# Kernel optimization log

Measured on AMD Instinct MI355X. Metric: run time of the kernel, lower is better.

The kernel has to match this reference:

```python
import jax, jax.numpy as jnp
import numpy as np

N = 6144          # num utterances (graph nodes)
D = 128           # utt_embed_size
WIN = 10          # att_window_size
NUM_SPK = 8
N_EMO = 7


def _init(key, shape):
    fan_in = shape[0]
    return jax.random.normal(key, shape, dtype=jnp.float32) * (1.0 / np.sqrt(fan_in))


def setup_inputs() -> dict:
    key = jax.random.key(0)
    ks = jax.random.split(key, 20)
    inp = {
        "x": jax.random.normal(ks[0], (N, D), dtype=jnp.float32),
        "speakers": jax.random.randint(ks[1], (N,), 0, NUM_SPK, dtype=jnp.int32),
        # layer-1 relation GCN weights (pred / suc / same / diff)
        "W_pred1": _init(ks[2], (D, D)),
        "W_suc1": _init(ks[3], (D, D)),
        "W_same1": _init(ks[4], (D, D)),
        "W_diff1": _init(ks[5], (D, D)),
        # layer-2 relation GCN weights
        "W_pred2": _init(ks[6], (D, D)),
        "W_suc2": _init(ks[7], (D, D)),
        "W_same2": _init(ks[8], (D, D)),
        "W_diff2": _init(ks[9], (D, D)),
        "w_aggr_1": _init(ks[10], (D, D)),
        "w_aggr_2": _init(ks[11], (D, D)),
        "w_e1": _init(ks[12], (2 * D, D)),
        "b_e1": jnp.zeros((D,), dtype=jnp.float32),
        "w_e2": _init(ks[13], (D, N_EMO)),
        "b_e2": jnp.zeros((N_EMO,), dtype=jnp.float32),
        "w_s": _init(ks[14], (2 * D, N_EMO)),
        "b_s": jnp.zeros((N_EMO,), dtype=jnp.float32),
    }
    return inp


def reference(x, speakers, W_pred1, W_suc1, W_same1, W_diff1,
              W_pred2, W_suc2, W_same2, W_diff2,
              w_aggr_1, w_aggr_2, w_e1, b_e1, w_e2, b_e2, w_s, b_s):
    n = x.shape[0]
    idx = jnp.arange(n)
    # windowed dot-product attention; entries outside the window stay 0.0
    # BEFORE the softmax (faithful to the torch code: zeros, not -inf)
    band = jnp.abs(idx[:, None] - idx[None, :]) <= WIN
    scores = jnp.where(band, x @ x.T, 0.0)            # [N, N]
    attn = jax.nn.softmax(scores, axis=1)
    # relation masks
    same = (speakers[:, None] == speakers[None, :]).astype(x.dtype)
    pred = (idx[None, :] >= idx[:, None]).astype(x.dtype)   # triu incl diag
    suc = 1.0 - pred                                          # strict lower tri
    adjs = (same * pred * attn,        # same-speaker, predecessor
            same * suc * attn,         # same-speaker, successor
            (1.0 - same) * pred * attn,  # diff-speaker, predecessor
            (1.0 - same) * suc * attn)   # diff-speaker, successor

    def gcn(h, Ws):  # sum_k adj_k @ (h @ W_k)
        return sum(a @ (h @ w) for a, w in zip(adjs, Ws))

    d = jnp.diagonal(attn)[:, None]   # self-attention scale
    h1 = jax.nn.relu(gcn(x, (W_pred1, W_suc1, W_same1, W_diff1))
                     + (x @ w_aggr_1) * d)
    h2 = jax.nn.relu(gcn(h1, (W_pred2, W_suc2, W_same2, W_diff2))
                     + (h1 @ w_aggr_2) * d)
    h = jnp.concatenate([h2, x], axis=1)              # [N, 2D]
    emotion = jax.nn.relu(h @ w_e1 + b_e1) @ w_e2 + b_e2   # [N, 7]
    sentiment = h @ w_s + b_s                               # [N, 7]
    return emotion, sentiment
```

## Files before the change

### kernel.cpp

```cpp
#include <hip/hip_runtime.h>
#include <hip/hip_bf16.h>


#define NN   6144
#define DD   128
#define WINW 10
#define YST  168
#define TAB_OFF 27456
#define SS_OFF  33088
#define SM_BYTES 35904
#define NBLK 768
#define WS_W1T 0
#define WS_W2T 163840
#define WS_WE1 327680
#define WS_WE2 393216
#define WS_WST 397312
#define WS_H1  405504
#define WS_H2  1978368
#define BAR_OFF 3551232
#define F1_OFF 16384
#define F2_OFF 40960
#define BAR_BYTES 65536

typedef unsigned short u16;
typedef unsigned long long u64;
typedef __attribute__((ext_vector_type(8))) short bf16x8;
typedef __attribute__((ext_vector_type(4))) float f32x4;

__device__ __forceinline__ float b2f(u16 u) {
    return __uint_as_float(((unsigned int)u) << 16);
}
__device__ __forceinline__ u16 f2b(float f) {
    __hip_bfloat16 h = __float2bfloat16(f);
    return *reinterpret_cast<u16*>(&h);
}
__device__ __forceinline__ bf16x8 cvt8(const float* p) {
    float4 u = *reinterpret_cast<const float4*>(p);
    float4 v = *reinterpret_cast<const float4*>(p + 4);
    bf16x8 r;
    r[0] = (short)f2b(u.x); r[1] = (short)f2b(u.y);
    r[2] = (short)f2b(u.z); r[3] = (short)f2b(u.w);
    r[4] = (short)f2b(v.x); r[5] = (short)f2b(v.y);
    r[6] = (short)f2b(v.z); r[7] = (short)f2b(v.w);
    return r;
}
__device__ __forceinline__ void st_agent_u32(unsigned* p, unsigned v) {
    __hip_atomic_store(p, v, __ATOMIC_RELAXED, __HIP_MEMORY_SCOPE_AGENT);
}
__device__ __forceinline__ void st_agent_u64(u64* p, u64 v) {
    __hip_atomic_store(p, v, __ATOMIC_RELAXED, __HIP_MEMORY_SCOPE_AGENT);
}
__device__ __forceinline__ unsigned ld_agent_u32(const unsigned* p) {
    return __hip_atomic_load(p, __ATOMIC_RELAXED, __HIP_MEMORY_SCOPE_AGENT);
}
__device__ __forceinline__ unsigned add_agent_u32(unsigned* p, unsigned v) {
    return __hip_atomic_fetch_add(p, v, __ATOMIC_RELAXED,
                                  __HIP_MEMORY_SCOPE_AGENT);
}
__device__ __forceinline__ void poll_ge(unsigned* p, unsigned v) {
    while (ld_agent_u32(p) < v) __builtin_amdgcn_s_sleep(1);
}
__device__ __forceinline__ const float* sel5(int r,
    const float* a0, const float* a1, const float* a2,
    const float* a3, const float* a4) {
    return r == 0 ? a0 : r == 1 ? a1 : r == 2 ? a2 : r == 3 ? a3 : a4;
}

__device__ __forceinline__ void layer_tile(
    const float* __restrict__ x, const u16* __restrict__ Ab16,
    const u16* __restrict__ BT, const int* __restrict__ spk,
    u16* __restrict__ hout, int first_layer, int hb, int bm,
    char* smraw, int tid, char* gate, int bid)
{
    u16*   Ys  = (u16*)smraw;
    float* Xs  = (float*)smraw;
    int2*  tab = (int2*)(smraw + TAB_OFF);
    float* Ss  = (float*)(smraw + SS_OFF);
    const int wave = tid >> 6, lane = tid & 63;
    const int lm = lane & 15, quad = lane >> 4;
    const int wm = wave >> 1, wn = wave & 1;

    bf16x8 afr[2][4];

    if (first_layer) {
        #pragma unroll
        for (int it = 0; it < 7; ++it) {
            int f = tid + it * 256;
            if (f < 52 * 32) {
                int s = f >> 5, c = f & 31;
                int g = min(max(bm - WINW + s, 0), NN - 1);
                *reinterpret_cast<float4*>(&Xs[s * 132 + c * 4]) =
                    *reinterpret_cast<const float4*>(&x[(size_t)g * DD + c * 4]);
            }
        }
        __syncthreads();

        if (tid < 128) {
            const int il = tid >> 2, q = tid & 3;
            const float* xr = &Xs[(il + WINW) * 132 + q * 32];
            float4 xq[8];
            #pragma unroll
            for (int c = 0; c < 8; ++c) {
                int cc = (c + 2 * q) & 7;
                xq[c] = *reinterpret_cast<const float4*>(xr + cc * 4);
            }
            float po[21];
            #pragma unroll
            for (int o = 0; o < 21; ++o) {
                const float* jr = &Xs[(il + o) * 132 + q * 32];
                float a0 = 0.f, a1 = 0.f, a2 = 0.f, a3 = 0.f;
                #pragma unroll
                for (int c = 0; c < 8; ++c) {
                    int cc = (c + 2 * q) & 7;
                    float4 b = *reinterpret_cast<const float4*>(jr + cc * 4);
                    a0 = fmaf(xq[c].x, b.x, a0); a1 = fmaf(xq[c].y, b.y, a1);
                    a2 = fmaf(xq[c].z, b.z, a2); a3 = fmaf(xq[c].w, b.w, a3);
                }
                po[o] = (a0 + a1) + (a2 + a3);
            }
            #pragma unroll
            for (int o = 0; o < 21; ++o) {
                po[o] += __shfl_xor(po[o], 1);
                po[o] += __shfl_xor(po[o], 2);
            }
            if (q == 0) {
                #pragma unroll
                for (int o = 0; o < 21; ++o) {
                    int jg = bm + il - WINW + o;
                    Ss[il * 22 + o] =
                        (jg >= 0 && jg < NN) ? po[o] : -1e30f;
                }
            }
        }
        __syncthreads();

        if (tid < 32) {
            int il = tid, i = bm + il;
            float m = 0.f;
            #pragma unroll
            for (int o = 0; o < 21; ++o) {
                float s = Ss[il * 22 + o];
                if (s > -1e29f) m = fmaxf(m, s);
            }
            int lo = i - WINW; if (lo < 0) lo = 0;
            int hi = i + WINW; if (hi > NN - 1) hi = NN - 1;
            float Z = (float)(NN - (hi - lo + 1)) * __expf(-m);
            float ev[21];
            #pragma unroll
            for (int o = 0; o < 21; ++o) {
                float s = Ss[il * 22 + o];
                ev[o] = (s > -1e29f) ? __expf(s - m) : 0.f;
                Z += ev[o];
            }
            float rz = 1.f / Z;
            #pragma unroll
            for (int o = 0; o < 21; ++o) Ss[il * 22 + o] = ev[o] * rz;
        }
        __syncthreads();

        #pragma unroll
        for (int rr = 0; rr < 3; ++rr) {
            int p = tid + rr * 256;
            if (p < 704) {
                int il = p / 22, e = p - il * 22;
                int i  = bm + il;
                int si = spk[i];
                float w; int off;
                if (e < 21) {
                    int j = i - WINW + e;
                    bool valid = (j >= 0) && (j < NN);
                    int jc  = valid ? j : i;
                    int sel = (spk[jc] == si) ? ((j >= i) ? 0 : 1)
                                              : ((j >= i) ? 2 : 3);
                    w   = valid ? Ss[il * 22 + e] : 0.f;
                    off = valid ? (il + e) * YST + sel * 32 : 0;
                } else {
                    w   = Ss[il * 22 + WINW];
                    off = (il + WINW) * YST + 4 * 32;
                }
                tab[p] = make_int2(__float_as_int(w), off);
            }
        }

        #pragma unroll
        for (int mt = 0; mt < 2; ++mt) {
            int rl = min((wm * 2 + mt) * 16 + lm, 51);
            #pragma unroll
            for (int s = 0; s < 4; ++s)
                afr[mt][s] = cvt8(&Xs[rl * 132 + s * 32 + quad * 8]);
        }
        __syncthreads();

        if (gate) {
            if (tid == 0) {
                unsigned g = (unsigned)bid >> 5;
                unsigned* gflag = (unsigned*)(gate + 8192 + g * 128);
                unsigned* rflag = (unsigned*)(gate + 12288);
                if ((bid & 31) == 0) {
                    poll_ge(rflag, 1u);
                    st_agent_u32(gflag, 1u);
                } else {
                    poll_ge(gflag, 1u);
                }
            }
            __syncthreads();
            __builtin_amdgcn_sched_barrier(0);
        }
    } else {
        #pragma unroll
        for (int mt = 0; mt < 2; ++mt) {
            int gr = min(max(bm - WINW + (wm * 2 + mt) * 16 + lm, 0), NN - 1);
            #pragma unroll
            for (int s = 0; s < 4; ++s)
                afr[mt][s] = *reinterpret_cast<const bf16x8*>(
                    Ab16 + (size_t)gr * DD + s * 32 + quad * 8);
        }
    }

    f32x4 acc[2][5];
    #pragma unroll
    for (int mt = 0; mt < 2; ++mt)
        #pragma unroll
        for (int n = 0; n < 5; ++n) acc[mt][n] = {0.f, 0.f, 0.f, 0.f};

    #pragma unroll
    for (int np = 0; np < 5; ++np) {
        int nt = wn * 5 + np;
        int gn = (nt >> 1) * 128 + hb * 32 + (nt & 1) * 16 + lm;
        #pragma unroll
        for (int s = 0; s < 4; ++s) {
            bf16x8 b = *reinterpret_cast<const bf16x8*>(
                BT + (size_t)gn * DD + s * 32 + quad * 8);
            acc[0][np] = __builtin_amdgcn_mfma_f32_16x16x32_bf16(afr[0][s], b, acc[0][np], 0, 0, 0);
            acc[1][np] = __builtin_amdgcn_mfma_f32_16x16x32_bf16(afr[1][s], b, acc[1][np], 0, 0, 0);
        }
    }
    #pragma unroll
    for (int mt = 0; mt < 2; ++mt)
        #pragma unroll
        for (int np = 0; np < 5; ++np) {
            int nt = wn * 5 + np;
            #pragma unroll
            for (int r = 0; r < 4; ++r) {
                int lr = (wm * 2 + mt) * 16 + quad * 4 + r;
                if (lr < 52) Ys[lr * YST + nt * 16 + lm] = f2b(acc[mt][np][r]);
            }
        }
    __syncthreads();

    const int c0 = (tid & 7) * 4;
    const int il = tid >> 3;
    {
        float a0 = 0.f, a1 = 0.f, a2 = 0.f, a3 = 0.f;
        const int2* tp = &tab[il * 22];
        #pragma unroll
        for (int e = 0; e < 22; ++e) {
            int2 t = tp[e];
            float w = __int_as_float(t.x);
            u64 y4 = *reinterpret_cast<const u64*>(Ys + t.y + c0);
            a0 = fmaf(w, b2f((u16)(y4 & 0xffff)), a0);
            a1 = fmaf(w, b2f((u16)((y4 >> 16) & 0xffff)), a1);
            a2 = fmaf(w, b2f((u16)((y4 >> 32) & 0xffff)), a2);
            a3 = fmaf(w, b2f((u16)(y4 >> 48)), a3);
        }
        int i = bm + il;
        u64 pk = (u64)f2b(fmaxf(a0, 0.f)) |
                 ((u64)f2b(fmaxf(a1, 0.f)) << 16) |
                 ((u64)f2b(fmaxf(a2, 0.f)) << 32) |
                 ((u64)f2b(fmaxf(a3, 0.f)) << 48);
        st_agent_u64(reinterpret_cast<u64*>(
            &hout[(size_t)i * DD + hb * 32 + c0]), pk);
    }
}

__global__ __launch_bounds__(256, 4) void fused_kernel(
    const float* __restrict__ x, const int* __restrict__ spk,
    const float* __restrict__ p0, const float* __restrict__ p1,
    const float* __restrict__ p2, const float* __restrict__ p3,
    const float* __restrict__ p4,
    const float* __restrict__ q0, const float* __restrict__ q1,
    const float* __restrict__ q2, const float* __restrict__ q3,
    const float* __restrict__ q4,
    const float* __restrict__ we1, const float* __restrict__ be1,
    const float* __restrict__ we2, const float* __restrict__ be2,
    const float* __restrict__ wss, const float* __restrict__ bss,
    float* __restrict__ out, char* __restrict__ ws)
{
    u16*   W1T   = (u16*)(ws + WS_W1T);
    u16*   W2T   = (u16*)(ws + WS_W2T);
    u16*   We1T  = (u16*)(ws + WS_WE1);
    u16*   we2T  = (u16*)(ws + WS_WE2);
    u16*   wsT   = (u16*)(ws + WS_WST);
    u16*   h1b   = (u16*)(ws + WS_H1);
    u16*   h2b   = (u16*)(ws + WS_H2);
    char*  bar   = ws + BAR_OFF;
    unsigned* flag1 = (unsigned*)(bar + F1_OFF);
    unsigned* flag2 = (unsigned*)(bar + F2_OFF);

    __shared__ __align__(16) char smraw[SM_BYTES];
    const int bid = blockIdx.x;
    const int tid = threadIdx.x;

    if (bid < 160) {
        unsigned* W1T32 = (unsigned*)W1T;
        unsigned* W2T32 = (unsigned*)W2T;
        int idx = bid * 256 + tid;
        int c = idx & 127, rk = idx >> 7;
        int r = rk >> 6, k2 = rk & 63, k = k2 * 2;
        const float* s1 = sel5(r, p0, p1, p2, p3, p4);
        const float* s2 = sel5(r, q0, q1, q2, q3, q4);
        unsigned v1 = (unsigned)f2b(s1[k * 128 + c]) |
                      ((unsigned)f2b(s1[(k + 1) * 128 + c]) << 16);
        unsigned v2 = (unsigned)f2b(s2[k * 128 + c]) |
                      ((unsigned)f2b(s2[(k + 1) * 128 + c]) << 16);
        int U = (r * 128 + c) * 64 + k2;
        st_agent_u32(&W1T32[U], v1);
        st_agent_u32(&W2T32[U], v2);
    } else if (bid < 192) {
        unsigned* We1T32 = (unsigned*)We1T;
        #pragma unroll
        for (int it = 0; it < 2; ++it) {
            int idx = (bid - 160) * 256 + tid + it * 8192;
            int n = idx & 127, k2 = idx >> 7, k = k2 * 2;
            unsigned v = (unsigned)f2b(we1[k * 128 + n]) |
                         ((unsigned)f2b(we1[(k + 1) * 128 + n]) << 16);
            st_agent_u32(&We1T32[n * 128 + k2], v);
        }
    } else if (bid == 192) {
        unsigned* we2T32 = (unsigned*)we2T;
        #pragma unroll
        for (int it = 0; it < 4; ++it) {
            int U = tid + it * 256;
            int n = U >> 6, kh = U & 63, k = kh * 2;
            float lo = n < 7 ? we2[k * 7 + n] : 0.f;
            float hi = n < 7 ? we2[(k + 1) * 7 + n] : 0.f;
            st_agent_u32(&we2T32[U],
                         (unsigned)f2b(lo) | ((unsigned)f2b(hi) << 16));
        }
    } else if (bid == 193) {
        unsigned* wsT32 = (unsigned*)wsT;
        #pragma unroll
        for (int it = 0; it < 8; ++it) {
            int U = tid + it * 256;
            int n = U >> 7, kh = U & 127, k = kh * 2;
            float lo = n < 7 ? wss[k * 7 + n] : 0.f;
            float hi = n < 7 ? wss[(k + 1) * 7 + n] : 0.f;
            st_agent_u32(&wsT32[U],
                         (unsigned)f2b(lo) | ((unsigned)f2b(hi) << 16));
        }
    }

    __syncthreads();
    if (tid == 0) {
        unsigned g = (unsigned)bid >> 5;
        unsigned* gctr = (unsigned*)(bar + g * 128);
        unsigned* rctr = (unsigned*)(bar + 4096);
        unsigned* rflag = (unsigned*)(bar + 12288);
        unsigned r = add_agent_u32(gctr, 1u);
        if (r == 31u) {
            unsigned rr = add_agent_u32(rctr, 1u);
            if (rr == 23u) st_agent_u32(rflag, 1u);
        }
    }

    const int hb = bid / 192, bmi = bid - hb * 192;
    const int bm = bmi * 32;
    layer_tile(x, nullptr, W1T, spk, h1b, 1, hb, bm, smraw, tid, bar, bid);

    __syncthreads();
    if (tid == 0) add_agent_u32(&flag1[bmi * 32], 1u);
    if (tid == 0) {
        if (bmi > 0)   poll_ge(&flag1[(bmi - 1) * 32], 4u);
        poll_ge(&flag1[bmi * 32], 4u);
        if (bmi < 191) poll_ge(&flag1[(bmi + 1) * 32], 4u);
    }
    __syncthreads();
    __builtin_amdgcn_sched_barrier(0);

    layer_tile(nullptr, h1b, W2T, spk, h2b, 0, hb, bm, smraw, tid, nullptr, bid);

    __syncthreads();
    if (tid == 0) add_agent_u32(&flag2[bmi * 32], 1u);

    if (bid < 384) {
        const int rt = (bid & ~15) | ((bid & 7) << 1) | ((bid >> 3) & 1);
        const int bmh = rt * 16;
        if (tid == 0) poll_ge(&flag2[(rt >> 1) * 32], 4u);
        __syncthreads();
        __builtin_amdgcn_sched_barrier(0);

        float* Es = (float*)smraw;
        const int wave = tid >> 6, lane = tid & 63;
        const int lm = lane & 15, quad = lane >> 4;
        const int row = bmh + lm;

        bf16x8 afr[8];
        #pragma unroll
        for (int s = 0; s < 4; ++s)
            afr[s] = *reinterpret_cast<const bf16x8*>(
                &h2b[(size_t)row * DD + s * 32 + quad * 8]);
        #pragma unroll
        for (int s = 4; s < 8; ++s)
            afr[s] = cvt8(&x[(size_t)row * DD + (s - 4) * 32 + quad * 8]);

        f32x4 accE[2], accS = {0.f, 0.f, 0.f, 0.f};
        #pragma unroll
        for (int n = 0; n < 2; ++n) accE[n] = {0.f, 0.f, 0.f, 0.f};

        #pragma unroll
        for (int s = 0; s < 8; ++s) {
            #pragma unroll
            for (int n = 0; n < 2; ++n) {
                int nt = wave * 2 + n;
                bf16x8 b = *reinterpret_cast<const bf16x8*>(
                    &We1T[(size_t)(nt * 16 + lm) * 256 + s * 32 + quad * 8]);
                accE[n] = __builtin_amdgcn_mfma_f32_16x16x32_bf16(afr[s], b, accE[n], 0, 0, 0);
            }
            if (wave == 0) {
                bf16x8 bsf = *reinterpret_cast<const bf16x8*>(
                    &wsT[(size_t)lm * 256 + s * 32 + quad * 8]);
                accS = __builtin_amdgcn_mfma_f32_16x16x32_bf16(afr[s], bsf, accS, 0, 0, 0);
            }
        }

        if (wave == 0 && lm < 7) {
            #pragma unroll
            for (int r = 0; r < 4; ++r) {
                int i = bmh + quad * 4 + r;
                out[(size_t)NN * 7 + (size_t)i * 7 + lm] = accS[r] + bss[lm];
            }
        }
        #pragma unroll
        for (int n = 0; n < 2; ++n) {
            int col = (wave * 2 + n) * 16 + lm;
            float bias = be1[col];
            #pragma unroll
            for (int r = 0; r < 4; ++r)
                Es[(quad * 4 + r) * 132 + col] = fmaxf(accE[n][r] + bias, 0.f);
        }
        __syncthreads();

        if (wave == 0) {
            f32x4 accM = {0.f, 0.f, 0.f, 0.f};
            #pragma unroll
            for (int s = 0; s < 4; ++s) {
                bf16x8 a = cvt8(&Es[lm * 132 + s * 32 + quad * 8]);
                bf16x8 b = *reinterpret_cast<const bf16x8*>(
                    &we2T[(size_t)lm * 128 + s * 32 + quad * 8]);
                accM = __builtin_amdgcn_mfma_f32_16x16x32_bf16(a, b, accM, 0, 0, 0);
            }
            if (lm < 7) {
                #pragma unroll
                for (int r = 0; r < 4; ++r) {
                    int i = bmh + quad * 4 + r;
                    out[(size_t)i * 7 + lm] = accM[r] + be2[lm];
                }
            }
        }
    }
}

extern "C" void kernel_launch(void* const* d_in, const int* in_sizes, int n_in,
                              void* d_out, int out_size, void* d_ws, size_t ws_size,
                              hipStream_t stream)
{
    const float* x   = (const float*)d_in[0];
    const int*   spk = (const int*)d_in[1];
    const float* Wp1 = (const float*)d_in[2];
    const float* Wu1 = (const float*)d_in[3];
    const float* Wm1 = (const float*)d_in[4];
    const float* Wd1 = (const float*)d_in[5];
    const float* Wp2 = (const float*)d_in[6];
    const float* Wu2 = (const float*)d_in[7];
    const float* Wm2 = (const float*)d_in[8];
    const float* Wd2 = (const float*)d_in[9];
    const float* wa1 = (const float*)d_in[10];
    const float* wa2 = (const float*)d_in[11];
    const float* we1 = (const float*)d_in[12];
    const float* be1 = (const float*)d_in[13];
    const float* we2 = (const float*)d_in[14];
    const float* be2 = (const float*)d_in[15];
    const float* wss = (const float*)d_in[16];
    const float* bss = (const float*)d_in[17];
    float* out = (float*)d_out;
    char*  ws  = (char*)d_ws;

    hipMemsetAsync(ws + BAR_OFF, 0, BAR_BYTES, stream);

    fused_kernel<<<dim3(NBLK), dim3(256), 0, stream>>>(
        x, spk, Wp1, Wu1, Wm1, Wd1, wa1, Wp2, Wu2, Wm2, Wd2, wa2,
        we1, be1, we2, be2, wss, bss, out, ws);
}
```

Before: 131.1 us.

## Shrink row tiles to 24 rows and launch 1024 blocks

Cuts the per-block row tile from 32 to 24 rows (44-row halo), raising the grid from 768 to 1024 blocks so more CUs are busy in the persistent fused kernel. The weight-pack readiness barrier is reduced to a single counter over the first 194 blocks instead of a hierarchical count over all blocks. The head-stage tile flags are remapped to the new tile size. In exchange, halo recomputation per useful row rises, and half the waves now issue only one MFMA row tile, so the matrix units are less evenly loaded.

```diff
diff --git a/kernel.cpp b/kernel.cpp
--- a/kernel.cpp
+++ b/kernel.cpp
@@ -5,11 +5,15 @@
 #define NN   6144
 #define DD   128
 #define WINW 10
+#define ROWS 24
+#define HALO 44
+#define NTIL 256
 #define YST  168
-#define TAB_OFF 27456
-#define SS_OFF  33088
-#define SM_BYTES 35904
-#define NBLK 768
+#define TAB_OFF 23232
+#define SS_OFF  27456
+#define SM_BYTES 29568
+#define NBLK 1024
+#define NPACK 194
 #define WS_W1T 0
 #define WS_W2T 163840
 #define WS_WE1 327680
@@ -19,8 +23,8 @@
 #define WS_H2  1978368
 #define BAR_OFF 3551232
 #define F1_OFF 16384
-#define F2_OFF 40960
-#define BAR_BYTES 65536
+#define F2_OFF 49152
+#define BAR_BYTES 81920
 
 typedef unsigned short u16;
 typedef unsigned long long u64;
@@ -79,14 +83,15 @@
     const int wave = tid >> 6, lane = tid & 63;
     const int lm = lane & 15, quad = lane >> 4;
     const int wm = wave >> 1, wn = wave & 1;
+    const int nmt = (wm == 0) ? 2 : 1;
 
     bf16x8 afr[2][4];
 
     if (first_layer) {
         #pragma unroll
-        for (int it = 0; it < 7; ++it) {
+        for (int it = 0; it < 6; ++it) {
             int f = tid + it * 256;
-            if (f < 52 * 32) {
+            if (f < HALO * 32) {
                 int s = f >> 5, c = f & 31;
                 int g = min(max(bm - WINW + s, 0), NN - 1);
                 *reinterpret_cast<float4*>(&Xs[s * 132 + c * 4]) =
@@ -95,15 +100,13 @@
         }
         __syncthreads();
 
-        if (tid < 128) {
+        if (tid < ROWS * 4) {
             const int il = tid >> 2, q = tid & 3;
             const float* xr = &Xs[(il + WINW) * 132 + q * 32];
             float4 xq[8];
             #pragma unroll
-            for (int c = 0; c < 8; ++c) {
-                int cc = (c + 2 * q) & 7;
-                xq[c] = *reinterpret_cast<const float4*>(xr + cc * 4);
-            }
+            for (int c = 0; c < 8; ++c)
+                xq[c] = *reinterpret_cast<const float4*>(xr + c * 4);
             float po[21];
             #pragma unroll
             for (int o = 0; o < 21; ++o) {
@@ -111,8 +114,7 @@
                 float a0 = 0.f, a1 = 0.f, a2 = 0.f, a3 = 0.f;
                 #pragma unroll
                 for (int c = 0; c < 8; ++c) {
-                    int cc = (c + 2 * q) & 7;
-                    float4 b = *reinterpret_cast<const float4*>(jr + cc * 4);
+                    float4 b = *reinterpret_cast<const float4*>(jr + c * 4);
                     a0 = fmaf(xq[c].x, b.x, a0); a1 = fmaf(xq[c].y, b.y, a1);
                     a2 = fmaf(xq[c].z, b.z, a2); a3 = fmaf(xq[c].w, b.w, a3);
                 }
@@ -134,7 +136,7 @@
         }
         __syncthreads();
 
-        if (tid < 32) {
+        if (tid < ROWS) {
             int il = tid, i = bm + il;
             float m = 0.f;
             #pragma unroll
@@ -161,7 +163,7 @@
         #pragma unroll
         for (int rr = 0; rr < 3; ++rr) {
             int p = tid + rr * 256;
-            if (p < 704) {
+            if (p < ROWS * 22) {
                 int il = p / 22, e = p - il * 22;
                 int i  = bm + il;
                 int si = spk[i];
@@ -182,9 +184,8 @@
             }
         }
 
-        #pragma unroll
-        for (int mt = 0; mt < 2; ++mt) {
-            int rl = min((wm * 2 + mt) * 16 + lm, 51);
+        for (int mt = 0; mt < nmt; ++mt) {
+            int rl = min((wm * 2 + mt) * 16 + lm, HALO - 1);
             #pragma unroll
             for (int s = 0; s < 4; ++s)
                 afr[mt][s] = cvt8(&Xs[rl * 132 + s * 32 + quad * 8]);
@@ -195,7 +196,7 @@
             if (tid == 0) {
                 unsigned g = (unsigned)bid >> 5;
                 unsigned* gflag = (unsigned*)(gate + 8192 + g * 128);
-                unsigned* rflag = (unsigned*)(gate + 12288);
+                unsigned* rflag = (unsigned*)(gate + 4096);
                 if ((bid & 31) == 0) {
                     poll_ge(rflag, 1u);
                     st_agent_u32(gflag, 1u);
@@ -207,8 +208,7 @@
             __builtin_amdgcn_sched_barrier(0);
         }
     } else {
-        #pragma unroll
-        for (int mt = 0; mt < 2; ++mt) {
+        for (int mt = 0; mt < nmt; ++mt) {
             int gr = min(max(bm - WINW + (wm * 2 + mt) * 16 + lm, 0), NN - 1);
             #pragma unroll
             for (int s = 0; s < 4; ++s)
@@ -232,25 +232,25 @@
             bf16x8 b = *reinterpret_cast<const bf16x8*>(
                 BT + (size_t)gn * DD + s * 32 + quad * 8);
             acc[0][np] = __builtin_amdgcn_mfma_f32_16x16x32_bf16(afr[0][s], b, acc[0][np], 0, 0, 0);
-            acc[1][np] = __builtin_amdgcn_mfma_f32_16x16x32_bf16(afr[1][s], b, acc[1][np], 0, 0, 0);
-        }
-    }
-    #pragma unroll
-    for (int mt = 0; mt < 2; ++mt)
+            if (wm == 0)
+                acc[1][np] = __builtin_amdgcn_mfma_f32_16x16x32_bf16(afr[1][s], b, acc[1][np], 0, 0, 0);
+        }
+    }
+    for (int mt = 0; mt < nmt; ++mt)
         #pragma unroll
         for (int np = 0; np < 5; ++np) {
             int nt = wn * 5 + np;
             #pragma unroll
             for (int r = 0; r < 4; ++r) {
                 int lr = (wm * 2 + mt) * 16 + quad * 4 + r;
-                if (lr < 52) Ys[lr * YST + nt * 16 + lm] = f2b(acc[mt][np][r]);
+                if (lr < HALO) Ys[lr * YST + nt * 16 + lm] = f2b(acc[mt][np][r]);
             }
         }
     __syncthreads();
 
-    const int c0 = (tid & 7) * 4;
-    const int il = tid >> 3;
-    {
+    if (tid < ROWS * 8) {
+        const int c0 = (tid & 7) * 4;
+        const int il = tid >> 3;
         float a0 = 0.f, a1 = 0.f, a2 = 0.f, a3 = 0.f;
         const int2* tp = &tab[il * 22];
         #pragma unroll
@@ -350,29 +350,26 @@
         }
     }
 
-    __syncthreads();
-    if (tid == 0) {
-        unsigned g = (unsigned)bid >> 5;
-        unsigned* gctr = (unsigned*)(bar + g * 128);
-        unsigned* rctr = (unsigned*)(bar + 4096);
-        unsigned* rflag = (unsigned*)(bar + 12288);
-        unsigned r = add_agent_u32(gctr, 1u);
-        if (r == 31u) {
-            unsigned rr = add_agent_u32(rctr, 1u);
-            if (rr == 23u) st_agent_u32(rflag, 1u);
-        }
-    }
-
-    const int hb = bid / 192, bmi = bid - hb * 192;
-    const int bm = bmi * 32;
+    if (bid < NPACK) {
+        __syncthreads();
+        if (tid == 0) {
+            unsigned* pctr  = (unsigned*)(bar);
+            unsigned* rflag = (unsigned*)(bar + 4096);
+            unsigned r = add_agent_u32(pctr, 1u);
+            if (r == NPACK - 1) st_agent_u32(rflag, 1u);
+        }
+    }
+
+    const int hb = bid >> 8, bmi = bid & 255;
+    const int bm = bmi * ROWS;
     layer_tile(x, nullptr, W1T, spk, h1b, 1, hb, bm, smraw, tid, bar, bid);
 
     __syncthreads();
     if (tid == 0) add_agent_u32(&flag1[bmi * 32], 1u);
     if (tid == 0) {
-        if (bmi > 0)   poll_ge(&flag1[(bmi - 1) * 32], 4u);
+        if (bmi > 0)        poll_ge(&flag1[(bmi - 1) * 32], 4u);
         poll_ge(&flag1[bmi * 32], 4u);
-        if (bmi < 191) poll_ge(&flag1[(bmi + 1) * 32], 4u);
+        if (bmi < NTIL - 1) poll_ge(&flag1[(bmi + 1) * 32], 4u);
     }
     __syncthreads();
     __builtin_amdgcn_sched_barrier(0);
@@ -383,9 +380,12 @@
     if (tid == 0) add_agent_u32(&flag2[bmi * 32], 1u);
 
     if (bid < 384) {
-        const int rt = (bid & ~15) | ((bid & 7) << 1) | ((bid >> 3) & 1);
-        const int bmh = rt * 16;
-        if (tid == 0) poll_ge(&flag2[(rt >> 1) * 32], 4u);
+        const int bmh = bid * 16;
+        const int t0 = bmh / ROWS, t1 = (bmh + 15) / ROWS;
+        if (tid == 0) {
+            poll_ge(&flag2[t0 * 32], 4u);
+            if (t1 != t0) poll_ge(&flag2[t1 * 32], 4u);
+        }
         __syncthreads();
         __builtin_amdgcn_sched_barrier(0);
 
```

Measured after the change: 199.3 us. 52.0% more time.
